# Kernel tuning notes

Measured on AMD Instinct MI355X. Metric: run time of the kernel, lower is better.

## Reference

```python
import jax, jax.numpy as jnp
import numpy as np

N_NODES = 100000
N_EDGES = 3200000
D_FEAT = 128
N_CLASSES = 40


def setup_inputs() -> dict:
    key = jax.random.key(0)
    k1, k2, k3, k4 = jax.random.split(key, 4)
    x = jax.random.normal(k1, (N_NODES, D_FEAT), dtype=jnp.float32)
    edge_index = jax.random.randint(k2, (2, N_EDGES), 0, N_NODES, dtype=jnp.int64)
    # torch.nn.Linear default init ~ U(-1/sqrt(fan_in), 1/sqrt(fan_in)); randn is fine for a numeric baseline
    W = jax.random.normal(k3, (N_CLASSES, D_FEAT), dtype=jnp.float32) * (1.0 / np.sqrt(D_FEAT))
    b = jax.random.normal(k4, (N_CLASSES,), dtype=jnp.float32) * 0.01
    return {"x": x, "edge_index": edge_index, "W": W, "b": b, "K": 2}


def _sgc_forward(x, edge_index, W, b, K):
    N = x.shape[0]
    loop = jnp.arange(N, dtype=edge_index.dtype)
    # Outer add_self_loops in SGC.forward, then gcn_norm inside SGConv adds
    # self-loops AGAIN (PyG default add_self_loops=True) -> two self-loops per node.
    row = jnp.concatenate([edge_index[0], loop, loop])
    col = jnp.concatenate([edge_index[1], loop, loop])
    # gcn_norm: deg over destination (col) with unit edge weights
    deg = jax.ops.segment_sum(jnp.ones_like(row, dtype=x.dtype), col, num_segments=N)
    dinv = jnp.where(deg > 0, deg ** -0.5, 0.0)
    norm = dinv[row] * dinv[col]  # [E+2N]
    for _ in range(K):
        # out[col] += norm * x[row]  (K-hop symmetric-normalized propagation)
        x = jax.ops.segment_sum(norm[:, None] * x[row], col, num_segments=N)
    logits = x @ W.T + b  # [N, C]
    return jax.nn.log_softmax(logits, axis=1)


def reference(x, edge_index, W, b, K):
    return _sgc_forward(x, edge_index, W, b, K)
```

## Files before the change

### kernel.cpp

```cpp
#include <hip/hip_runtime.h>
#include <hip/hip_bf16.h>
#include <math.h>

#define DF 128
#define NC 40
#define GST 64
#define RB 8
#define RSZ 256
#define CHUNK 4096
#define CAP 12288

__device__ __forceinline__ float bf2f(unsigned short h) {
  unsigned int u = ((unsigned int)h) << 16;
  union { unsigned int u; float f; } c; c.u = u; return c.f;
}
__device__ __forceinline__ unsigned short f2bf(float x) {
  union { float f; unsigned int u; } c; c.f = x;
  unsigned int u = c.u;
  return (unsigned short)((u + 0x7fffu + ((u >> 16) & 1u)) >> 16);
}

__global__ __launch_bounds__(512) void k_binB(
    const int* __restrict__ row, const int* __restrict__ col,
    int* __restrict__ cnt, unsigned int* __restrict__ slab, int E, int NB) {
  __shared__ int hist[512];
  __shared__ int cursor[512];
  int t = threadIdx.x;
  if (t < NB) hist[t] = 0;
  __syncthreads();
  int s = blockIdx.x * CHUNK, e = min(E, s + CHUNK);
  for (int i = s + t; i < e; i += 512) atomicAdd(&hist[col[i] >> RB], 1);
  __syncthreads();
  if (t < NB) cursor[t] = hist[t] ? atomicAdd(&cnt[t], hist[t]) : 0;
  __syncthreads();
  for (int i = s + t; i < e; i += 512) {
    int c = col[i];
    int b = c >> RB;
    int p = atomicAdd(&cursor[b], 1);
    slab[(size_t)b * CAP + p] = ((unsigned int)row[i] << RB) | (unsigned int)(c & (RSZ - 1));
  }
}

__global__ __launch_bounds__(512) void k_bucket_scan(
    const int* __restrict__ cnt, int* __restrict__ base,
    int* __restrict__ off, int NB, int N, int E) {
  __shared__ int s[512];
  int t = threadIdx.x;
  int v = (t < NB) ? cnt[t] : 0;
  s[t] = v;
  __syncthreads();
  for (int o = 1; o < 512; o <<= 1) {
    int u = (t >= o) ? s[t - o] : 0;
    __syncthreads();
    s[t] += u;
    __syncthreads();
  }
  if (t < NB) base[t] = s[t] - v;
  if (t == 0) { base[NB] = E; off[N] = E; }
}

__global__ __launch_bounds__(512) void k_binC(
    const unsigned int* __restrict__ slab, const int* __restrict__ base,
    int* __restrict__ off, int* __restrict__ eidx, float* __restrict__ dinv, int N) {
  __shared__ int hist[RSZ];
  __shared__ int sc[RSZ];
  __shared__ int cur[RSZ];
  int b = blockIdx.x;
  int t = threadIdx.x;
  if (t < RSZ) hist[t] = 0;
  __syncthreads();
  int cb = base[b], ce = base[b + 1];
  int cnt_b = ce - cb;
  const unsigned int* src = slab + (size_t)b * CAP;
  for (int i = t; i < cnt_b; i += 512) atomicAdd(&hist[src[i] & (RSZ - 1)], 1);
  __syncthreads();
  int v = (t < RSZ) ? hist[t] : 0;
  if (t < RSZ) sc[t] = v;
  __syncthreads();
  for (int o = 1; o < RSZ; o <<= 1) {
    int u = (t < RSZ && t >= o) ? sc[t - o] : 0;
    __syncthreads();
    if (t < RSZ) sc[t] += u;
    __syncthreads();
  }
  if (t < RSZ) {
    int pos = cb + sc[t] - v;
    int node = (b << RB) + t;
    if (node < N) {
      off[node] = pos;
      dinv[node] = rsqrtf((float)v + 2.0f);
    }
    cur[t] = pos;
  }
  __syncthreads();
  for (int i = t; i < cnt_b; i += 512) {
    unsigned int en = src[i];
    int p = atomicAdd(&cur[en & (RSZ - 1)], 1);
    eidx[p] = (int)(en >> RB);
  }
}

__global__ __launch_bounds__(128) void k_xw_scale(
    const float* __restrict__ x, const float* __restrict__ W,
    const float* __restrict__ dinv, unsigned short* __restrict__ g0, int N) {
  __shared__ float4 Ws[NC * (DF / 4)];
  for (int i = threadIdx.x; i < NC * (DF / 4); i += blockDim.x)
    Ws[i] = ((const float4*)W)[i];
  __syncthreads();
  int node = blockIdx.x * blockDim.x + threadIdx.x;
  if (node >= N) return;
  float acc[NC];
#pragma unroll
  for (int c = 0; c < NC; ++c) acc[c] = 0.f;
  const float4* xr = (const float4*)(x + (size_t)node * DF);
#pragma unroll 1
  for (int ch = 0; ch < 8; ++ch) {
    float4 v0 = xr[ch * 4 + 0];
    float4 v1 = xr[ch * 4 + 1];
    float4 v2 = xr[ch * 4 + 2];
    float4 v3 = xr[ch * 4 + 3];
#pragma unroll
    for (int c = 0; c < NC; ++c) {
      float4 w0 = Ws[c * (DF / 4) + ch * 4 + 0];
      float4 w1 = Ws[c * (DF / 4) + ch * 4 + 1];
      float4 w2 = Ws[c * (DF / 4) + ch * 4 + 2];
      float4 w3 = Ws[c * (DF / 4) + ch * 4 + 3];
      acc[c] += (v0.x * w0.x + v0.y * w0.y + v0.z * w0.z + v0.w * w0.w) +
                (v1.x * w1.x + v1.y * w1.y + v1.z * w1.z + v1.w * w1.w) +
                (v2.x * w2.x + v2.y * w2.y + v2.z * w2.z + v2.w * w2.w) +
                (v3.x * w3.x + v3.y * w3.y + v3.z * w3.z + v3.w * w3.w);
    }
  }
  float di = dinv[node];
  unsigned int* gp = (unsigned int*)(g0 + (size_t)node * GST);
#pragma unroll
  for (int c2 = 0; c2 < NC / 2; ++c2) {
    unsigned int lo = f2bf(di * acc[c2 * 2 + 0]);
    unsigned int hi = f2bf(di * acc[c2 * 2 + 1]);
    gp[c2] = lo | (hi << 16);
  }
}

__global__ __launch_bounds__(256) void k_hop_mid(
    const int* __restrict__ off, const int* __restrict__ eidx,
    const float* __restrict__ dinv, const unsigned short* __restrict__ gin,
    unsigned short* __restrict__ gout, int N) {
  int wave = (int)((blockIdx.x * (size_t)blockDim.x + threadIdx.x) >> 6);
  int lane = threadIdx.x & 63;
  if (wave >= N) return;
  int node = wave;
  int s = __builtin_amdgcn_readfirstlane(off[node]);
  int e = __builtin_amdgcn_readfirstlane(off[node + 1]);
  const unsigned short* gl = gin + lane;
  float acc = 2.0f * bf2f(gl[(size_t)node * GST]);
  int i = s;
  for (; i + 8 <= e; i += 8) {
    int r0 = eidx[i + 0], r1 = eidx[i + 1], r2 = eidx[i + 2], r3 = eidx[i + 3];
    int r4 = eidx[i + 4], r5 = eidx[i + 5], r6 = eidx[i + 6], r7 = eidx[i + 7];
    unsigned short a0 = gl[(size_t)r0 * GST];
    unsigned short a1 = gl[(size_t)r1 * GST];
    unsigned short a2 = gl[(size_t)r2 * GST];
    unsigned short a3 = gl[(size_t)r3 * GST];
    unsigned short a4 = gl[(size_t)r4 * GST];
    unsigned short a5 = gl[(size_t)r5 * GST];
    unsigned short a6 = gl[(size_t)r6 * GST];
    unsigned short a7 = gl[(size_t)r7 * GST];
    acc += ((bf2f(a0) + bf2f(a1)) + (bf2f(a2) + bf2f(a3))) +
           ((bf2f(a4) + bf2f(a5)) + (bf2f(a6) + bf2f(a7)));
  }
  for (; i < e; ++i) acc += bf2f(gl[(size_t)eidx[i] * GST]);
  float di = dinv[node];
  gout[(size_t)node * GST + lane] = f2bf(di * di * acc);
}

__global__ __launch_bounds__(256) void k_hop_final(
    const int* __restrict__ off, const int* __restrict__ eidx,
    const float* __restrict__ dinv, const unsigned short* __restrict__ gin,
    const float* __restrict__ bias, float* __restrict__ out, int N) {
  int wave = (int)((blockIdx.x * (size_t)blockDim.x + threadIdx.x) >> 6);
  int lane = threadIdx.x & 63;
  if (wave >= N) return;
  int node = wave;
  int s = __builtin_amdgcn_readfirstlane(off[node]);
  int e = __builtin_amdgcn_readfirstlane(off[node + 1]);
  const unsigned short* gl = gin + lane;
  float acc = 2.0f * bf2f(gl[(size_t)node * GST]);
  int i = s;
  for (; i + 8 <= e; i += 8) {
    int r0 = eidx[i + 0], r1 = eidx[i + 1], r2 = eidx[i + 2], r3 = eidx[i + 3];
    int r4 = eidx[i + 4], r5 = eidx[i + 5], r6 = eidx[i + 6], r7 = eidx[i + 7];
    unsigned short a0 = gl[(size_t)r0 * GST];
    unsigned short a1 = gl[(size_t)r1 * GST];
    unsigned short a2 = gl[(size_t)r2 * GST];
    unsigned short a3 = gl[(size_t)r3 * GST];
    unsigned short a4 = gl[(size_t)r4 * GST];
    unsigned short a5 = gl[(size_t)r5 * GST];
    unsigned short a6 = gl[(size_t)r6 * GST];
    unsigned short a7 = gl[(size_t)r7 * GST];
    acc += ((bf2f(a0) + bf2f(a1)) + (bf2f(a2) + bf2f(a3))) +
           ((bf2f(a4) + bf2f(a5)) + (bf2f(a6) + bf2f(a7)));
  }
  for (; i < e; ++i) acc += bf2f(gl[(size_t)eidx[i] * GST]);
  float di = dinv[node];
  bool act = lane < NC;
  float v = act ? (di * acc + bias[lane]) : -3.0e38f;
  float m = v;
#pragma unroll
  for (int o = 32; o > 0; o >>= 1) m = fmaxf(m, __shfl_xor(m, o, 64));
  float ex = act ? expf(v - m) : 0.f;
  float ssum = ex;
#pragma unroll
  for (int o = 32; o > 0; o >>= 1) ssum += __shfl_xor(ssum, o, 64);
  float lse = m + logf(ssum);
  if (act) out[(size_t)node * NC + lane] = v - lse;
}

extern "C" void kernel_launch(void* const* d_in, const int* in_sizes, int n_in,
                              void* d_out, int out_size, void* d_ws, size_t ws_size,
                              hipStream_t stream) {
  const float* x = (const float*)d_in[0];
  const int* ei  = (const int*)d_in[1];
  const float* W = (const float*)d_in[2];
  const float* b = (const float*)d_in[3];
  float* out = (float*)d_out;

  const int N = in_sizes[0] / DF;
  const int E = in_sizes[1] / 2;
  const int NB = (N + RSZ - 1) >> RB;
  const int* row  = ei;
  const int* colv = ei + E;

  char* basep = (char*)d_ws;
  auto alloc = [&](size_t bytes) {
    char* p = basep;
    basep += (bytes + 511) & ~(size_t)511;
    return p;
  };
  int*   cnt    = (int*)  alloc(((size_t)NB) * 4);
  int*   bbase  = (int*)  alloc(((size_t)NB + 1) * 4);
  unsigned int* slab = (unsigned int*)alloc((size_t)NB * CAP * 4);
  int*   off    = (int*)  alloc(((size_t)N + 1) * 4);
  int*   eidx   = (int*)  alloc((size_t)E * 4);
  float* dinv   = (float*)alloc((size_t)N * 4);
  unsigned short* g0 = (unsigned short*)alloc((size_t)N * GST * 2);
  unsigned short* g1 = (unsigned short*)alloc((size_t)N * GST * 2);

  const int B = 256;
  const int gBin = (E + CHUNK - 1) / CHUNK;

  hipMemsetAsync(cnt, 0, (size_t)NB * 4, stream);
  k_binB<<<gBin, 512, 0, stream>>>(row, colv, cnt, slab, E, NB);
  k_bucket_scan<<<1, 512, 0, stream>>>(cnt, bbase, off, NB, N, E);
  k_binC<<<NB, 512, 0, stream>>>(slab, bbase, off, eidx, dinv, N);

  k_xw_scale<<<(N + 127) / 128, 128, 0, stream>>>(x, W, dinv, g0, N);

  const int gWave = (int)(((size_t)N * 64 + B - 1) / B);
  k_hop_mid  <<<gWave, B, 0, stream>>>(off, eidx, dinv, g0, g1, N);
  k_hop_final<<<gWave, B, 0, stream>>>(off, eidx, dinv, g1, b, out, N);
}
```

Measured before the change: 351.1 us.

## Shrink bf16 row stride to 40, mask idle lanes, deepen gather unroll, stage cols in LDS

The row stride of the projected bf16 feature buffer drops from 64 to 40 elements (80 bytes), so the rows are stored packed with no padding and the buffer is smaller. The hop kernels now gather only with the 40 active lanes. The gather loop is unrolled to 16 neighbors, with a 4-wide remainder loop, to keep more loads in flight. The binning kernel stages each chunk's column indices in shared memory so they are read from global memory once instead of twice. Risks: rows are no longer aligned to 128 bytes, so gathered rows can straddle cache lines, and the wider unroll raises register pressure.

Result: faster. 325.7 us (-7.2%).

```diff
diff --git a/kernel.cpp b/kernel.cpp
--- a/kernel.cpp
+++ b/kernel.cpp
@@ -4,7 +4,7 @@
 
 #define DF 128
 #define NC 40
-#define GST 64
+#define GST 40
 #define RB 8
 #define RSZ 256
 #define CHUNK 4096
@@ -23,21 +23,23 @@
 __global__ __launch_bounds__(512) void k_binB(
     const int* __restrict__ row, const int* __restrict__ col,
     int* __restrict__ cnt, unsigned int* __restrict__ slab, int E, int NB) {
+  __shared__ int colS[CHUNK];
   __shared__ int hist[512];
   __shared__ int cursor[512];
   int t = threadIdx.x;
   if (t < NB) hist[t] = 0;
-  __syncthreads();
-  int s = blockIdx.x * CHUNK, e = min(E, s + CHUNK);
-  for (int i = s + t; i < e; i += 512) atomicAdd(&hist[col[i] >> RB], 1);
+  int s = blockIdx.x * CHUNK, e = min(E, s + CHUNK), n = e - s;
+  for (int i = t; i < n; i += 512) colS[i] = col[s + i];
+  __syncthreads();
+  for (int i = t; i < n; i += 512) atomicAdd(&hist[colS[i] >> RB], 1);
   __syncthreads();
   if (t < NB) cursor[t] = hist[t] ? atomicAdd(&cnt[t], hist[t]) : 0;
   __syncthreads();
-  for (int i = s + t; i < e; i += 512) {
-    int c = col[i];
+  for (int i = t; i < n; i += 512) {
+    int c = colS[i];
     int b = c >> RB;
     int p = atomicAdd(&cursor[b], 1);
-    slab[(size_t)b * CAP + p] = ((unsigned int)row[i] << RB) | (unsigned int)(c & (RSZ - 1));
+    slab[(size_t)b * CAP + p] = ((unsigned int)row[s + i] << RB) | (unsigned int)(c & (RSZ - 1));
   }
 }
 
@@ -132,14 +134,36 @@
     }
   }
   float di = dinv[node];
-  unsigned int* gp = (unsigned int*)(g0 + (size_t)node * GST);
+  unsigned int pk[NC / 2];
 #pragma unroll
   for (int c2 = 0; c2 < NC / 2; ++c2) {
     unsigned int lo = f2bf(di * acc[c2 * 2 + 0]);
     unsigned int hi = f2bf(di * acc[c2 * 2 + 1]);
-    gp[c2] = lo | (hi << 16);
-  }
-}
+    pk[c2] = lo | (hi << 16);
+  }
+  uint4* gp = (uint4*)(g0 + (size_t)node * GST);
+#pragma unroll
+  for (int q = 0; q < 5; ++q)
+    gp[q] = make_uint4(pk[q * 4 + 0], pk[q * 4 + 1], pk[q * 4 + 2], pk[q * 4 + 3]);
+}
+
+#define GATHER16                                                        \
+    int r0 = eidx[i + 0], r1 = eidx[i + 1], r2 = eidx[i + 2], r3 = eidx[i + 3];   \
+    int r4 = eidx[i + 4], r5 = eidx[i + 5], r6 = eidx[i + 6], r7 = eidx[i + 7];   \
+    int r8 = eidx[i + 8], r9 = eidx[i + 9], rA = eidx[i + 10], rB = eidx[i + 11]; \
+    int rC = eidx[i + 12], rD = eidx[i + 13], rE = eidx[i + 14], rF = eidx[i + 15]; \
+    unsigned short a0 = gl[(size_t)r0 * GST]; unsigned short a1 = gl[(size_t)r1 * GST]; \
+    unsigned short a2 = gl[(size_t)r2 * GST]; unsigned short a3 = gl[(size_t)r3 * GST]; \
+    unsigned short a4 = gl[(size_t)r4 * GST]; unsigned short a5 = gl[(size_t)r5 * GST]; \
+    unsigned short a6 = gl[(size_t)r6 * GST]; unsigned short a7 = gl[(size_t)r7 * GST]; \
+    unsigned short a8 = gl[(size_t)r8 * GST]; unsigned short a9 = gl[(size_t)r9 * GST]; \
+    unsigned short aA = gl[(size_t)rA * GST]; unsigned short aB = gl[(size_t)rB * GST]; \
+    unsigned short aC = gl[(size_t)rC * GST]; unsigned short aD = gl[(size_t)rD * GST]; \
+    unsigned short aE = gl[(size_t)rE * GST]; unsigned short aF = gl[(size_t)rF * GST]; \
+    acc += (((bf2f(a0) + bf2f(a1)) + (bf2f(a2) + bf2f(a3))) +           \
+            ((bf2f(a4) + bf2f(a5)) + (bf2f(a6) + bf2f(a7)))) +          \
+           (((bf2f(a8) + bf2f(a9)) + (bf2f(aA) + bf2f(aB))) +           \
+            ((bf2f(aC) + bf2f(aD)) + (bf2f(aE) + bf2f(aF))));
 
 __global__ __launch_bounds__(256) void k_hop_mid(
     const int* __restrict__ off, const int* __restrict__ eidx,
@@ -151,26 +175,23 @@
   int node = wave;
   int s = __builtin_amdgcn_readfirstlane(off[node]);
   int e = __builtin_amdgcn_readfirstlane(off[node + 1]);
-  const unsigned short* gl = gin + lane;
-  float acc = 2.0f * bf2f(gl[(size_t)node * GST]);
-  int i = s;
-  for (; i + 8 <= e; i += 8) {
-    int r0 = eidx[i + 0], r1 = eidx[i + 1], r2 = eidx[i + 2], r3 = eidx[i + 3];
-    int r4 = eidx[i + 4], r5 = eidx[i + 5], r6 = eidx[i + 6], r7 = eidx[i + 7];
-    unsigned short a0 = gl[(size_t)r0 * GST];
-    unsigned short a1 = gl[(size_t)r1 * GST];
-    unsigned short a2 = gl[(size_t)r2 * GST];
-    unsigned short a3 = gl[(size_t)r3 * GST];
-    unsigned short a4 = gl[(size_t)r4 * GST];
-    unsigned short a5 = gl[(size_t)r5 * GST];
-    unsigned short a6 = gl[(size_t)r6 * GST];
-    unsigned short a7 = gl[(size_t)r7 * GST];
-    acc += ((bf2f(a0) + bf2f(a1)) + (bf2f(a2) + bf2f(a3))) +
-           ((bf2f(a4) + bf2f(a5)) + (bf2f(a6) + bf2f(a7)));
-  }
-  for (; i < e; ++i) acc += bf2f(gl[(size_t)eidx[i] * GST]);
-  float di = dinv[node];
-  gout[(size_t)node * GST + lane] = f2bf(di * di * acc);
+  if (lane < NC) {
+    const unsigned short* gl = gin + lane;
+    float acc = 2.0f * bf2f(gl[(size_t)node * GST]);
+    int i = s;
+    for (; i + 16 <= e; i += 16) { GATHER16 }
+    for (; i + 4 <= e; i += 4) {
+      int r0 = eidx[i + 0], r1 = eidx[i + 1], r2 = eidx[i + 2], r3 = eidx[i + 3];
+      unsigned short a0 = gl[(size_t)r0 * GST];
+      unsigned short a1 = gl[(size_t)r1 * GST];
+      unsigned short a2 = gl[(size_t)r2 * GST];
+      unsigned short a3 = gl[(size_t)r3 * GST];
+      acc += (bf2f(a0) + bf2f(a1)) + (bf2f(a2) + bf2f(a3));
+    }
+    for (; i < e; ++i) acc += bf2f(gl[(size_t)eidx[i] * GST]);
+    float di = dinv[node];
+    gout[(size_t)node * GST + lane] = f2bf(di * di * acc);
+  }
 }
 
 __global__ __launch_bounds__(256) void k_hop_final(
@@ -183,26 +204,24 @@
   int node = wave;
   int s = __builtin_amdgcn_readfirstlane(off[node]);
   int e = __builtin_amdgcn_readfirstlane(off[node + 1]);
-  const unsigned short* gl = gin + lane;
-  float acc = 2.0f * bf2f(gl[(size_t)node * GST]);
-  int i = s;
-  for (; i + 8 <= e; i += 8) {
-    int r0 = eidx[i + 0], r1 = eidx[i + 1], r2 = eidx[i + 2], r3 = eidx[i + 3];
-    int r4 = eidx[i + 4], r5 = eidx[i + 5], r6 = eidx[i + 6], r7 = eidx[i + 7];
-    unsigned short a0 = gl[(size_t)r0 * GST];
-    unsigned short a1 = gl[(size_t)r1 * GST];
-    unsigned short a2 = gl[(size_t)r2 * GST];
-    unsigned short a3 = gl[(size_t)r3 * GST];
-    unsigned short a4 = gl[(size_t)r4 * GST];
-    unsigned short a5 = gl[(size_t)r5 * GST];
-    unsigned short a6 = gl[(size_t)r6 * GST];
-    unsigned short a7 = gl[(size_t)r7 * GST];
-    acc += ((bf2f(a0) + bf2f(a1)) + (bf2f(a2) + bf2f(a3))) +
-           ((bf2f(a4) + bf2f(a5)) + (bf2f(a6) + bf2f(a7)));
-  }
-  for (; i < e; ++i) acc += bf2f(gl[(size_t)eidx[i] * GST]);
+  float acc = 0.f;
+  bool act = lane < NC;
+  if (act) {
+    const unsigned short* gl = gin + lane;
+    acc = 2.0f * bf2f(gl[(size_t)node * GST]);
+    int i = s;
+    for (; i + 16 <= e; i += 16) { GATHER16 }
+    for (; i + 4 <= e; i += 4) {
+      int r0 = eidx[i + 0], r1 = eidx[i + 1], r2 = eidx[i + 2], r3 = eidx[i + 3];
+      unsigned short a0 = gl[(size_t)r0 * GST];
+      unsigned short a1 = gl[(size_t)r1 * GST];
+      unsigned short a2 = gl[(size_t)r2 * GST];
+      unsigned short a3 = gl[(size_t)r3 * GST];
+      acc += (bf2f(a0) + bf2f(a1)) + (bf2f(a2) + bf2f(a3));
+    }
+    for (; i < e; ++i) acc += bf2f(gl[(size_t)eidx[i] * GST]);
+  }
   float di = dinv[node];
-  bool act = lane < NC;
   float v = act ? (di * acc + bias[lane]) : -3.0e38f;
   float m = v;
 #pragma unroll
```
